# Kernel tuning notes

Hardware: AMD Instinct MI355X
Metric: run time of the kernel (lower is better)

## Reference

```python
import jax, jax.numpy as jnp
import numpy as np

DIM = 512
HEADS = 16
HIDDEN = 2048
EPS = 1e-5


def _layernorm(x, g, b):
    mu = jnp.mean(x, axis=-1, keepdims=True)
    var = jnp.mean((x - mu) ** 2, axis=-1, keepdims=True)
    return (x - mu) * jax.lax.rsqrt(var + EPS) * g + b


def _heads_merge(o):
    # Faithful to source: sum.reshape(B, N, D) applied to [B, H, N, pd]
    # WITHOUT transposing heads back (reproduces the original bug).
    B, H, N, pd = o.shape
    return o.reshape(B, N, H * pd)


def _self_attn(x, w, b, H):
    B, N, D = x.shape
    pd = D // H
    qkv = (x @ w + b).reshape(B, N, 3, H, pd).transpose(2, 0, 3, 1, 4)
    q, k, v = qkv[0], qkv[1], qkv[2]
    # NOTE: no 1/sqrt(pd) scaling in the source.
    s = jax.nn.softmax(jnp.einsum('bhnd,bhmd->bhnm', q, k), axis=-1)
    o = jnp.einsum('bhnm,bhmd->bhnd', s, v)  # == broadcast-multiply-and-sum in source
    return _heads_merge(o)


def _cross_attn(x1, x2, qw, qb, kvw, kvb, H):
    B, N, D = x1.shape
    pd = D // H
    q = (x2 @ qw + qb).reshape(B, N, H, pd).transpose(0, 2, 1, 3)
    kv = (x1 @ kvw + kvb).reshape(B, N, 2, H, pd).transpose(2, 0, 3, 1, 4)
    k, v = kv[0], kv[1]
    s = jax.nn.softmax(jnp.einsum('bhnd,bhmd->bhnm', q, k), axis=-1)
    o = jnp.einsum('bhnm,bhmd->bhnd', s, v)
    return _heads_merge(o)


def setup_inputs() -> dict:
    key = jax.random.key(0)
    ks = jax.random.split(key, 16)
    B, N, D, Hd = 4, 2048, DIM, HIDDEN
    s = 0.02
    return {
        'x1': jax.random.normal(ks[0], (B, N, D), jnp.float32),
        'x2': jax.random.normal(ks[1], (B, N, D), jnp.float32),
        'qkv_w': jax.random.normal(ks[2], (D, 3 * D), jnp.float32) * s,
        'qkv_b': jnp.zeros((3 * D,), jnp.float32),
        'q_w': jax.random.normal(ks[3], (D, D), jnp.float32) * s,
        'q_b': jnp.zeros((D,), jnp.float32),
        'kv_w': jax.random.normal(ks[4], (D, 2 * D), jnp.float32) * s,
        'kv_b': jnp.zeros((2 * D,), jnp.float32),
        'norm_g': jnp.ones((D,), jnp.float32),
        'norm_b': jnp.zeros((D,), jnp.float32),
        'fc1_w': jax.random.normal(ks[5], (D, Hd), jnp.float32) * s,
        'fc1_b': jnp.zeros((Hd,), jnp.float32),
        'fc2_w': jax.random.normal(ks[6], (Hd, D), jnp.float32) * s,
        'fc2_b': jnp.zeros((D,), jnp.float32),
    }


def reference(x1, x2, qkv_w, qkv_b, q_w, q_b, kv_w, kv_b, norm_g, norm_b,
              fc1_w, fc1_b, fc2_w, fc2_b):
    # CrossSelfDecoder.forward
    x = x2 + _cross_attn(x1, x2, q_w, q_b, kv_w, kv_b, HEADS)
    n = _layernorm(x, norm_g, norm_b)  # same norm params reused (as in source)
    x = n + _self_attn(n, qkv_w, qkv_b, HEADS)
    n = _layernorm(x, norm_g, norm_b)
    h = jax.nn.gelu(n @ fc1_w + fc1_b, approximate=False)
    x = n + (h @ fc2_w + fc2_b)
    return x
```

## Files before the change

kernel.cpp:

```cpp
#include <hip/hip_runtime.h>
#include <math.h>

#define DIM 512
#define HEADS 16
#define PD 32
#define NSEQ 2048
#define BATCH 4
#define HIDDEN 2048
#define LOG2E 1.44269504088896f

typedef __attribute__((ext_vector_type(8))) __bf16 bf16x8;
typedef __attribute__((ext_vector_type(4))) float f32x4;
typedef __attribute__((ext_vector_type(16))) float f32x16;

__device__ __forceinline__ ushort f2bf(float f) {
    unsigned u = __float_as_uint(f);
    u = (u + 0x7FFFu + ((u >> 16) & 1u)) >> 16;
    return (ushort)u;
}

__device__ __forceinline__ unsigned cvtpk_bf16(float lo, float hi) {
    unsigned r;
    asm("v_cvt_pk_bf16_f32 %0, %1, %2" : "=v"(r) : "v"(lo), "v"(hi));
    return r;
}

__device__ __forceinline__ float exp2_fast(float x) {
    float r;
    asm("v_exp_f32 %0, %1" : "=v"(r) : "v"(x));
    return r;
}

typedef __attribute__((address_space(1))) const unsigned int g_u32;
typedef __attribute__((address_space(3))) unsigned int l_u32;
__device__ __forceinline__ void gload16(const void* g, void* l) {
    __builtin_amdgcn_global_load_lds((g_u32*)g, (l_u32*)l, 16, 0, 0);
}

__device__ __forceinline__ float gelu_exact(float v) {
    return 0.5f * v * (1.0f + erff(v * 0.70710678118654752f));
}

__global__ __launch_bounds__(256)
void tr_all_kernel(const float* __restrict__ q_w, const float* __restrict__ kv_w,
                   const float* __restrict__ qkv_w, const float* __restrict__ fc1_w,
                   const float* __restrict__ fc2_w, ushort* __restrict__ wtb,
                   const float* __restrict__ x1, const float* __restrict__ x2,
                   ushort* __restrict__ x1b, ushort* __restrict__ x2b)
{
    const int bid = blockIdx.x;
    if (bid >= 3584) {
        int cb = bid - 3584;
        const float* src = (cb < 2048) ? x1 : x2;
        ushort* dst = (cb < 2048) ? x1b : x2b;
        size_t base = (size_t)(cb & 2047) * 2048 + threadIdx.x * 8;
        float4 f0 = *(const float4*)&src[base];
        float4 f1 = *(const float4*)&src[base + 4];
        union { ushort u[8]; uint4 v; } t;
        t.u[0] = f2bf(f0.x); t.u[1] = f2bf(f0.y); t.u[2] = f2bf(f0.z); t.u[3] = f2bf(f0.w);
        t.u[4] = f2bf(f1.x); t.u[5] = f2bf(f1.y); t.u[6] = f2bf(f1.z); t.u[7] = f2bf(f1.w);
        *(uint4*)&dst[base] = t.v;
        return;
    }
    __shared__ float t[32][33];
    const float* W; ushort* Wt; int K, N, lb;
    if (bid < 256)       { W = q_w;   Wt = wtb;           K = 512;  N = 512;  lb = bid; }
    else if (bid < 768)  { W = kv_w;  Wt = wtb + 262144;  K = 512;  N = 1024; lb = bid - 256; }
    else if (bid < 1536) { W = qkv_w; Wt = wtb + 786432;  K = 512;  N = 1536; lb = bid - 768; }
    else if (bid < 2560) { W = fc1_w; Wt = wtb + 1572864; K = 512;  N = 2048; lb = bid - 1536; }
    else                 { W = fc2_w; Wt = wtb + 2621440; K = 2048; N = 512;  lb = bid - 2560; }
    const int nx = N / 32;
    const int n0 = (lb % nx) * 32, k0 = (lb / nx) * 32;
    const int tid = threadIdx.x;
    const int c = tid & 31, r0 = tid >> 5;
    #pragma unroll
    for (int i = 0; i < 4; ++i) {
        int r = r0 + i * 8;
        t[r][c] = W[(size_t)(k0 + r) * N + n0 + c];
    }
    __syncthreads();
    #pragma unroll
    for (int i = 0; i < 4; ++i) {
        int r = r0 + i * 8;
        Wt[(size_t)(n0 + r) * K + k0 + c] = f2bf(t[c][r]);
    }
}

template<int EPI, int NT>
__global__ __launch_bounds__(256)
void mgemm_bf(const ushort* __restrict__ Ap, const ushort* __restrict__ Bt,
              const float* __restrict__ bias, const float* __restrict__ resp,
              void* __restrict__ Cp, ushort* __restrict__ vtp,
              int M, int K, int Nc, int qcols, int vcol0)
{
    const int BN = 32 * NT;
    __shared__ __align__(16) ushort As[2][128 * 32];
    __shared__ __align__(16) ushort Bs[2][BN * 32];

    const int tid = threadIdx.x;
    const int wid = tid >> 6, ln = tid & 63;
    const int g = ln >> 4, c = ln & 15;
    const int wr = wid >> 1, wc = wid & 1;

    const int nwg = gridDim.x * gridDim.y;
    const int lid = blockIdx.y * gridDim.x + blockIdx.x;
    const int wg  = (lid & 7) * (nwg >> 3) + (lid >> 3);
    const int by = wg / gridDim.x, bx = wg % gridDim.x;
    const int row0 = by * 128, col0 = bx * BN;

    const f32x4 fzero = {0.f, 0.f, 0.f, 0.f};
    f32x4 acc[4][NT];
    #pragma unroll
    for (int i = 0; i < 4; ++i)
        #pragma unroll
        for (int j = 0; j < NT; ++j) acc[i][j] = fzero;

    const ushort* asrc[2];
    const ushort* bsrc[NT / 2];
    #pragma unroll
    for (int i = 0; i < 2; ++i) {
        int p = i * 256 + wid * 64 + ln;
        int row = p >> 2;
        int q4 = (p & 3) ^ ((row >> 1) & 3);
        asrc[i] = Ap + (size_t)(row0 + row) * K + q4 * 8;
    }
    #pragma unroll
    for (int i = 0; i < NT / 2; ++i) {
        int p = i * 256 + wid * 64 + ln;
        int row = p >> 2;
        int q4 = (p & 3) ^ ((row >> 1) & 3);
        bsrc[i] = Bt + (size_t)(col0 + row) * K + q4 * 8;
    }

    auto gstage = [&](int bi, int kk) {
        #pragma unroll
        for (int i = 0; i < 2; ++i)
            gload16(asrc[i] + kk, &As[bi][(i * 256 + wid * 64) * 8]);
        #pragma unroll
        for (int i = 0; i < NT / 2; ++i)
            gload16(bsrc[i] + kk, &Bs[bi][(i * 256 + wid * 64) * 8]);
    };

    const int ps = (c >> 1) & 3;
    const int nk = K / 32;

    gstage(0, 0);

    for (int ks = 0; ks < nk; ++ks) {
        __syncthreads();
        if (ks + 1 < nk) gstage((ks + 1) & 1, (ks + 1) * 32);
        const ushort* Ab = As[ks & 1];
        const ushort* Bb = Bs[ks & 1];

        bf16x8 a[4], b[NT];
        #pragma unroll
        for (int mt = 0; mt < 4; ++mt)
            a[mt] = *(const bf16x8*)&Ab[(wr * 64 + mt * 16 + c) * 32 + ((g ^ ps) * 8)];
        #pragma unroll
        for (int nt = 0; nt < NT; ++nt)
            b[nt] = *(const bf16x8*)&Bb[(wc * (16 * NT) + nt * 16 + c) * 32 + ((g ^ ps) * 8)];

        #pragma unroll
        for (int mt = 0; mt < 4; ++mt)
            #pragma unroll
            for (int nt = 0; nt < NT; ++nt)
                acc[mt][nt] = __builtin_amdgcn_mfma_f32_16x16x32_bf16(a[mt], b[nt], acc[mt][nt], 0, 0, 0);
    }

    float bs[NT];
    #pragma unroll
    for (int nt = 0; nt < NT; ++nt) bs[nt] = bias[col0 + wc * (16 * NT) + nt * 16 + c];

    #pragma unroll
    for (int mt = 0; mt < 4; ++mt) {
        const int rb = row0 + wr * 64 + mt * 16 + g * 4;
        #pragma unroll
        for (int nt = 0; nt < NT; ++nt) {
            const int col = col0 + wc * (16 * NT) + nt * 16 + c;
            if (EPI == 3 && col >= vcol0) {
                int cc = col - vcol0;
                int hh = cc >> 5, pd = cc & 31;
                int bq = rb >> 11, ntok = rb & 2047;
                union { ushort u[4]; uint2 v; } pk;
                #pragma unroll
                for (int reg = 0; reg < 4; ++reg)
                    pk.u[reg] = f2bf(acc[mt][nt][reg] + bs[nt]);
                *(uint2*)&vtp[((size_t)(bq * 16 + hh) * 32 + pd) * 2048 + ntok] = pk.v;
            } else {
                #pragma unroll
                for (int reg = 0; reg < 4; ++reg) {
                    int r = rb + reg;
                    float v = acc[mt][nt][reg] + bs[nt];
                    if (EPI == 1) {
                        ((ushort*)Cp)[(size_t)r * Nc + col] = f2bf(gelu_exact(v));
                    } else if (EPI == 2) {
                        ((float*)Cp)[(size_t)r * Nc + col] = v + resp[(size_t)r * Nc + col];
                    } else {
                        float v2 = (col < qcols) ? v * LOG2E : v;
                        ((ushort*)Cp)[(size_t)r * Nc + col] = f2bf(v2);
                    }
                }
            }
        }
    }
}

__global__ __launch_bounds__(256)
void attn_mfma_kernel(const ushort* __restrict__ qb_, int qstride, int qoff,
                      const ushort* __restrict__ kb_, int kstride, int koff,
                      const ushort* __restrict__ vtg,
                      const float* res, const float* __restrict__ gptr,
                      const float* __restrict__ bptr,
                      float* nf32, ushort* __restrict__ nb16)
{
    __shared__ __align__(16) ushort Klds[2][128 * 32];
    __shared__ __align__(16) ushort Vtlds[2][32 * 128];

    const int tid = threadIdx.x;
    const int w   = tid >> 6;
    const int ln  = tid & 63;
    const int c32 = ln & 31;
    const int hi  = ln >> 5;

    const int bid = blockIdx.x;
    const int xcd = bid & 7, jj = bid >> 3;
    const int bh = xcd + 8 * (jj >> 4);
    const int qt = jj & 15;
    const int b = bh >> 4, h = bh & 15;
    const size_t rowbase = (size_t)b * NSEQ;
    const int qt0 = qt * 128 + w * 32;
    const int n = qt0 + c32;

    bf16x8 qfrag[2];
    #pragma unroll
    for (int ph = 0; ph < 2; ++ph)
        qfrag[ph] = *(const bf16x8*)(qb_ + (rowbase + n) * qstride + qoff
                                     + h * PD + ph * 16 + hi * 8);

    const ushort* ks[2];
    const ushort* vs[2];
    int kd[2], vd[2];
    #pragma unroll
    for (int i = 0; i < 2; ++i) {
        int ch = 2 * w + i;
        int kvc = ch * 16 + (ln >> 2);
        int q4  = (ln & 3) ^ ((kvc >> 1) & 3);
        ks[i] = kb_ + (rowbase + kvc) * kstride + koff + h * PD + q4 * 8;
        kd[i] = ch * 512;
        int pdc = ch * 4 + (ln >> 4);
        int kv0 = ((ln & 15) ^ (pdc & 15)) * 8;
        vs[i] = vtg + ((size_t)bh * PD + pdc) * 2048 + kv0;
        vd[i] = ch * 512;
    }

#define STAGE(bi, trow)                                              \
    {                                                                \
        gload16(ks[0] + (size_t)(trow) * kstride, &Klds[bi][kd[0]]); \
        gload16(ks[1] + (size_t)(trow) * kstride, &Klds[bi][kd[1]]); \
        gload16(vs[0] + (trow), &Vtlds[bi][vd[0]]);                  \
        gload16(vs[1] + (trow), &Vtlds[bi][vd[1]]);                  \
    }

    f32x16 oacc, zero16;
    #pragma unroll
    for (int i = 0; i < 16; ++i) { oacc[i] = 0.f; zero16[i] = 0.f; }
    float l = 0.f;

    STAGE(0, 0);

    for (int t = 0; t < NSEQ / 128; ++t) {
        __syncthreads();
        if (t < NSEQ / 128 - 1) STAGE((t + 1) & 1, (t + 1) * 128);
        const ushort* Kb = Klds[t & 1];
        const ushort* Vb = Vtlds[t & 1];

        #pragma unroll
        for (int hh = 0; hh < 2; ++hh) {
            bf16x8 kf[2][2];
            #pragma unroll
            for (int kt = 0; kt < 2; ++kt)
                #pragma unroll
                for (int ph = 0; ph < 2; ++ph) {
                    int slot = (2 * ph + hi) ^ ((c32 >> 1) & 3);
                    kf[kt][ph] = *(const bf16x8*)&Kb[(hh * 64 + kt * 32 + c32) * 32 + slot * 8];
                }
            bf16x8 vf[4];
            #pragma unroll
            for (int j = 0; j < 4; ++j) {
                int slot = (hh * 8 + 2 * j + hi) ^ (c32 & 15);
                vf[j] = *(const bf16x8*)&Vb[c32 * 128 + slot * 8];
            }

            f32x16 st[2];
            __builtin_amdgcn_s_setprio(1);
            #pragma unroll
            for (int kt = 0; kt < 2; ++kt) {
                st[kt] = __builtin_amdgcn_mfma_f32_32x32x16_bf16(kf[kt][0], qfrag[0], zero16, 0, 0, 0);
                st[kt] = __builtin_amdgcn_mfma_f32_32x32x16_bf16(kf[kt][1], qfrag[1], st[kt], 0, 0, 0);
            }
            __builtin_amdgcn_s_setprio(0);

            float r0 = 0.f, r1 = 0.f, r2 = 0.f, r3 = 0.f;
            #pragma unroll
            for (int kt = 0; kt < 2; ++kt) {
                #pragma unroll
                for (int i = 0; i < 4; ++i) {
                    float p0 = exp2_fast(st[kt][i * 4 + 0]);
                    float p1 = exp2_fast(st[kt][i * 4 + 1]);
                    float p2 = exp2_fast(st[kt][i * 4 + 2]);
                    float p3 = exp2_fast(st[kt][i * 4 + 3]);
                    st[kt][i * 4 + 0] = p0; r0 += p0;
                    st[kt][i * 4 + 1] = p1; r1 += p1;
                    st[kt][i * 4 + 2] = p2; r2 += p2;
                    st[kt][i * 4 + 3] = p3; r3 += p3;
                }
            }
            float rsum = (r0 + r1) + (r2 + r3);
            rsum += __shfl_xor(rsum, 32);
            l += rsum;

            unsigned wpk[2][4][2];
            #pragma unroll
            for (int kt = 0; kt < 2; ++kt)
                #pragma unroll
                for (int rg = 0; rg < 4; ++rg) {
                    wpk[kt][rg][0] = cvtpk_bf16(st[kt][rg * 4 + 0], st[kt][rg * 4 + 1]);
                    wpk[kt][rg][1] = cvtpk_bf16(st[kt][rg * 4 + 2], st[kt][rg * 4 + 3]);
                }

            __builtin_amdgcn_s_setprio(1);
            #pragma unroll
            for (int j = 0; j < 4; ++j) {
                int kt = j >> 1, rg0 = 2 * (j & 1);
                unsigned x0 = wpk[kt][rg0][0], y0 = wpk[kt][rg0 + 1][0];
                unsigned x1 = wpk[kt][rg0][1], y1 = wpk[kt][rg0 + 1][1];
                asm("v_permlane32_swap_b32 %0, %1" : "+v"(x0), "+v"(y0));
                asm("v_permlane32_swap_b32 %0, %1" : "+v"(x1), "+v"(y1));
                union { unsigned u[4]; bf16x8 v; } pf;
                pf.u[0] = x0; pf.u[1] = x1; pf.u[2] = y0; pf.u[3] = y1;
                oacc = __builtin_amdgcn_mfma_f32_32x32x16_bf16(vf[j], pf.v, oacc, 0, 0, 0);
            }
            __builtin_amdgcn_s_setprio(0);
        }
    }
#undef STAGE

    const float inv = 1.0f / l;
    const int row2 = h * 128 + (n >> 4);
    const int colb = (n & 15) * PD;
    const size_t rowoff = (rowbase + row2) * DIM;

    float xv[16];
    float s = 0.f, ss = 0.f;
    #pragma unroll
    for (int ch = 0; ch < 4; ++ch) {
        float4 r4 = *(const float4*)&res[rowoff + colb + ch * 8 + hi * 4];
        #pragma unroll
        for (int q = 0; q < 4; ++q) {
            float rv = (q == 0) ? r4.x : (q == 1) ? r4.y : (q == 2) ? r4.z : r4.w;
            float x = rv + oacc[ch * 4 + q] * inv;
            xv[ch * 4 + q] = x; s += x; ss += x * x;
        }
    }
    s += __shfl_xor(s, 1);  ss += __shfl_xor(ss, 1);
    s += __shfl_xor(s, 2);  ss += __shfl_xor(ss, 2);
    s += __shfl_xor(s, 4);  ss += __shfl_xor(ss, 4);
    s += __shfl_xor(s, 8);  ss += __shfl_xor(ss, 8);
    s += __shfl_xor(s, 32); ss += __shfl_xor(ss, 32);
    float mu = s * (1.0f / DIM);
    float var = ss * (1.0f / DIM) - mu * mu;
    float rr = rsqrtf(var + 1e-5f);

    #pragma unroll
    for (int ch = 0; ch < 4; ++ch) {
        const int off = colb + ch * 8 + hi * 4;
        float4 g4 = *(const float4*)&gptr[off];
        float4 b4 = *(const float4*)&bptr[off];
        float y0 = (xv[ch * 4 + 0] - mu) * rr * g4.x + b4.x;
        float y1 = (xv[ch * 4 + 1] - mu) * rr * g4.y + b4.y;
        float y2 = (xv[ch * 4 + 2] - mu) * rr * g4.z + b4.z;
        float y3 = (xv[ch * 4 + 3] - mu) * rr * g4.w + b4.w;
        float4 yv = {y0, y1, y2, y3};
        *(float4*)&nf32[rowoff + off] = yv;
        uint2 pk = {cvtpk_bf16(y0, y1), cvtpk_bf16(y2, y3)};
        *(uint2*)&nb16[rowoff + off] = pk;
    }
}

extern "C" void kernel_launch(void* const* d_in, const int* in_sizes, int n_in,
                              void* d_out, int out_size, void* d_ws, size_t ws_size,
                              hipStream_t stream)
{
    const float* x1     = (const float*)d_in[0];
    const float* x2     = (const float*)d_in[1];
    const float* qkv_w  = (const float*)d_in[2];
    const float* qkv_b  = (const float*)d_in[3];
    const float* q_w    = (const float*)d_in[4];
    const float* q_b    = (const float*)d_in[5];
    const float* kv_w   = (const float*)d_in[6];
    const float* kv_b   = (const float*)d_in[7];
    const float* norm_g = (const float*)d_in[8];
    const float* norm_b = (const float*)d_in[9];
    const float* fc1_w  = (const float*)d_in[10];
    const float* fc1_b  = (const float*)d_in[11];
    const float* fc2_w  = (const float*)d_in[12];
    const float* fc2_b  = (const float*)d_in[13];
    float* out = (float*)d_out;
    float* ws  = (float*)d_ws;

    const int M = BATCH * NSEQ;
    const int BIG = 1 << 30;

    ushort* wtb    = (ushort*)ws;
    ushort* q_wt   = wtb;
    ushort* kv_wt  = wtb + 262144;
    ushort* qkv_wt = wtb + 786432;
    ushort* fc1_wt = wtb + 1572864;
    ushort* fc2_wt = wtb + 2621440;
    ushort* proj_u = (ushort*)(ws + (size_t)2 * 1024 * 1024);
    ushort* kvb16  = proj_u;
    ushort* qb16   = proj_u + (size_t)8192 * 1024;
    ushort* qkvb16 = proj_u;
    ushort* hbuf   = proj_u;
    ushort* VtG    = (ushort*)(ws + (size_t)21 * 512 * 1024);
    float*  n1f32  = ws + (size_t)13 * 1024 * 1024;
    ushort* n1b16  = (ushort*)(ws + (size_t)17 * 1024 * 1024);
    ushort* n2b16  = (ushort*)(ws + (size_t)19 * 1024 * 1024);
    ushort* x1b    = n1b16;
    ushort* x2b    = n2b16;

    dim3 blk(256);

    tr_all_kernel<<<dim3(7680), blk, 0, stream>>>(
        q_w, kv_w, qkv_w, fc1_w, fc2_w, wtb, x1, x2, x1b, x2b);

    mgemm_bf<3, 4><<<dim3(1024 / 128, M / 128), blk, 0, stream>>>(
        x1b, kv_wt, kv_b, nullptr, kvb16, VtG, M, DIM, 1024, 0, 512);
    mgemm_bf<3, 2><<<dim3(512 / 64, M / 128), blk, 0, stream>>>(
        x2b, q_wt, q_b, nullptr, qb16, nullptr, M, DIM, 512, 512, BIG);
    attn_mfma_kernel<<<dim3(1024), blk, 0, stream>>>(
        qb16, 512, 0, kvb16, 1024, 0, VtG, x2, norm_g, norm_b, n1f32, n1b16);

    mgemm_bf<3, 4><<<dim3(1536 / 128, M / 128), blk, 0, stream>>>(
        n1b16, qkv_wt, qkv_b, nullptr, qkvb16, VtG, M, DIM, 1536, 512, 1024);
    attn_mfma_kernel<<<dim3(1024), blk, 0, stream>>>(
        qkvb16, 1536, 0, qkvb16, 1536, 512, VtG, n1f32, norm_g, norm_b, n1f32, n2b16);

    mgemm_bf<1, 4><<<dim3(HIDDEN / 128, M / 128), blk, 0, stream>>>(
        n2b16, fc1_wt, fc1_b, nullptr, hbuf, nullptr, M, DIM, HIDDEN, 0, BIG);
    mgemm_bf<2, 2><<<dim3(512 / 64, M / 128), blk, 0, stream>>>(
        hbuf, fc2_wt, fc2_b, n1f32, out, nullptr, M, HIDDEN, DIM, 0, BIG);
}
```

Before: 274.2 us.

## Split attention over two KV halves and merge with separate layernorm kernel

```diff
diff --git a/kernel.cpp b/kernel.cpp
--- a/kernel.cpp
+++ b/kernel.cpp
@@ -17,6 +17,10 @@
     unsigned u = __float_as_uint(f);
     u = (u + 0x7FFFu + ((u >> 16) & 1u)) >> 16;
     return (ushort)u;
+}
+
+__device__ __forceinline__ float bf2f(ushort u) {
+    return __uint_as_float(((unsigned)u) << 16);
 }
 
 __device__ __forceinline__ unsigned cvtpk_bf16(float lo, float hi) {
@@ -206,12 +210,10 @@
 }
 
 __global__ __launch_bounds__(256)
-void attn_mfma_kernel(const ushort* __restrict__ qb_, int qstride, int qoff,
+void attn_part_kernel(const ushort* __restrict__ qb_, int qstride, int qoff,
                       const ushort* __restrict__ kb_, int kstride, int koff,
                       const ushort* __restrict__ vtg,
-                      const float* res, const float* __restrict__ gptr,
-                      const float* __restrict__ bptr,
-                      float* nf32, ushort* __restrict__ nb16)
+                      ushort* __restrict__ opart, float* __restrict__ lpart)
 {
     __shared__ __align__(16) ushort Klds[2][128 * 32];
     __shared__ __align__(16) ushort Vtlds[2][32 * 128];
@@ -223,13 +225,19 @@
     const int hi  = ln >> 5;
 
     const int bid = blockIdx.x;
-    const int xcd = bid & 7, jj = bid >> 3;
+    const int half = bid >> 10;
+    const int sb = bid & 1023;
+    const int xcd = sb & 7, jj = sb >> 3;
     const int bh = xcd + 8 * (jj >> 4);
     const int qt = jj & 15;
     const int b = bh >> 4, h = bh & 15;
     const size_t rowbase = (size_t)b * NSEQ;
     const int qt0 = qt * 128 + w * 32;
     const int n = qt0 + c32;
+    const int t0base = half * (NSEQ / 2);
+
+    ushort* oph = opart + (size_t)half * 8192 * 512;
+    float*  lph = lpart + (size_t)half * 64 * 2048;
 
     bf16x8 qfrag[2];
     #pragma unroll
@@ -245,11 +253,11 @@
         int ch = 2 * w + i;
         int kvc = ch * 16 + (ln >> 2);
         int q4  = (ln & 3) ^ ((kvc >> 1) & 3);
-        ks[i] = kb_ + (rowbase + kvc) * kstride + koff + h * PD + q4 * 8;
+        ks[i] = kb_ + (rowbase + t0base + kvc) * kstride + koff + h * PD + q4 * 8;
         kd[i] = ch * 512;
         int pdc = ch * 4 + (ln >> 4);
         int kv0 = ((ln & 15) ^ (pdc & 15)) * 8;
-        vs[i] = vtg + ((size_t)bh * PD + pdc) * 2048 + kv0;
+        vs[i] = vtg + ((size_t)bh * PD + pdc) * 2048 + t0base + kv0;
         vd[i] = ch * 512;
     }
 
@@ -268,9 +276,9 @@
 
     STAGE(0, 0);
 
-    for (int t = 0; t < NSEQ / 128; ++t) {
+    for (int t = 0; t < NSEQ / 256; ++t) {
         __syncthreads();
-        if (t < NSEQ / 128 - 1) STAGE((t + 1) & 1, (t + 1) * 128);
+        if (t < NSEQ / 256 - 1) STAGE((t + 1) & 1, (t + 1) * 128);
         const ushort* Kb = Klds[t & 1];
         const ushort* Vb = Vtlds[t & 1];
 
@@ -345,46 +353,85 @@
     }
 #undef STAGE
 
-    const float inv = 1.0f / l;
     const int row2 = h * 128 + (n >> 4);
     const int colb = (n & 15) * PD;
     const size_t rowoff = (rowbase + row2) * DIM;
-
-    float xv[16];
+    #pragma unroll
+    for (int ch = 0; ch < 4; ++ch) {
+        const int off = colb + ch * 8 + hi * 4;
+        uint2 pk = {cvtpk_bf16(oacc[ch * 4 + 0], oacc[ch * 4 + 1]),
+                    cvtpk_bf16(oacc[ch * 4 + 2], oacc[ch * 4 + 3])};
+        *(uint2*)&oph[rowoff + off] = pk;
+    }
+    if (hi == 0) lph[(size_t)bh * 2048 + n] = l;
+}
+
+__global__ __launch_bounds__(256)
+void merge_ln_kernel(const ushort* __restrict__ opart, const float* __restrict__ lpart,
+                     const float* __restrict__ res, const float* __restrict__ gptr,
+                     const float* __restrict__ bptr,
+                     float* __restrict__ nf32, ushort* __restrict__ nb16)
+{
+    const int w = threadIdx.x >> 6, ln = threadIdx.x & 63;
+    const int r = blockIdx.x * 4 + w;
+    const int b = r >> 11, row2 = r & 2047, h = row2 >> 7;
+    const int col0 = ln * 8;
+    const int nn = (row2 & 127) * 16 + (col0 >> 5);
+    const size_t li = (size_t)(b * 16 + h) * 2048 + nn;
+    const float inv = 1.0f / (lpart[li] + lpart[li + 64 * 2048]);
+    const size_t oi = (size_t)r * 512 + col0;
+
+    uint4 o1 = *(const uint4*)&opart[oi];
+    uint4 o2 = *(const uint4*)&opart[oi + (size_t)8192 * 512];
+    float4 rs0 = *(const float4*)&res[oi];
+    float4 rs1 = *(const float4*)&res[oi + 4];
+
+    float x[8];
+    const unsigned* u1 = (const unsigned*)&o1;
+    const unsigned* u2 = (const unsigned*)&o2;
+    #pragma unroll
+    for (int j = 0; j < 4; ++j) {
+        float a0 = bf2f((ushort)(u1[j] & 0xFFFF)) + bf2f((ushort)(u2[j] & 0xFFFF));
+        float a1 = bf2f((ushort)(u1[j] >> 16))    + bf2f((ushort)(u2[j] >> 16));
+        float rv0 = (j < 2) ? ((j == 0) ? rs0.x : rs0.z) : ((j == 2) ? rs1.x : rs1.z);
+        float rv1 = (j < 2) ? ((j == 0) ? rs0.y : rs0.w) : ((j == 2) ? rs1.y : rs1.w);
+        x[j * 2 + 0] = rv0 + a0 * inv;
+        x[j * 2 + 1] = rv1 + a1 * inv;
+    }
+
     float s = 0.f, ss = 0.f;
     #pragma unroll
-    for (int ch = 0; ch < 4; ++ch) {
-        float4 r4 = *(const float4*)&res[rowoff + colb + ch * 8 + hi * 4];
-        #pragma unroll
-        for (int q = 0; q < 4; ++q) {
-            float rv = (q == 0) ? r4.x : (q == 1) ? r4.y : (q == 2) ? r4.z : r4.w;
-            float x = rv + oacc[ch * 4 + q] * inv;
-            xv[ch * 4 + q] = x; s += x; ss += x * x;
-        }
-    }
-    s += __shfl_xor(s, 1);  ss += __shfl_xor(ss, 1);
-    s += __shfl_xor(s, 2);  ss += __shfl_xor(ss, 2);
-    s += __shfl_xor(s, 4);  ss += __shfl_xor(ss, 4);
-    s += __shfl_xor(s, 8);  ss += __shfl_xor(ss, 8);
-    s += __shfl_xor(s, 32); ss += __shfl_xor(ss, 32);
+    for (int j = 0; j < 8; ++j) { s += x[j]; ss += x[j] * x[j]; }
+    #pragma unroll
+    for (int off = 1; off <= 32; off <<= 1) {
+        s  += __shfl_xor(s, off);
+        ss += __shfl_xor(ss, off);
+    }
     float mu = s * (1.0f / DIM);
     float var = ss * (1.0f / DIM) - mu * mu;
     float rr = rsqrtf(var + 1e-5f);
 
-    #pragma unroll
-    for (int ch = 0; ch < 4; ++ch) {
-        const int off = colb + ch * 8 + hi * 4;
-        float4 g4 = *(const float4*)&gptr[off];
-        float4 b4 = *(const float4*)&bptr[off];
-        float y0 = (xv[ch * 4 + 0] - mu) * rr * g4.x + b4.x;
-        float y1 = (xv[ch * 4 + 1] - mu) * rr * g4.y + b4.y;
-        float y2 = (xv[ch * 4 + 2] - mu) * rr * g4.z + b4.z;
-        float y3 = (xv[ch * 4 + 3] - mu) * rr * g4.w + b4.w;
-        float4 yv = {y0, y1, y2, y3};
-        *(float4*)&nf32[rowoff + off] = yv;
-        uint2 pk = {cvtpk_bf16(y0, y1), cvtpk_bf16(y2, y3)};
-        *(uint2*)&nb16[rowoff + off] = pk;
-    }
+    float4 g0 = *(const float4*)&gptr[col0];
+    float4 g1 = *(const float4*)&gptr[col0 + 4];
+    float4 b0 = *(const float4*)&bptr[col0];
+    float4 b1 = *(const float4*)&bptr[col0 + 4];
+    float y[8];
+    y[0] = (x[0] - mu) * rr * g0.x + b0.x;
+    y[1] = (x[1] - mu) * rr * g0.y + b0.y;
+    y[2] = (x[2] - mu) * rr * g0.z + b0.z;
+    y[3] = (x[3] - mu) * rr * g0.w + b0.w;
+    y[4] = (x[4] - mu) * rr * g1.x + b1.x;
+    y[5] = (x[5] - mu) * rr * g1.y + b1.y;
+    y[6] = (x[6] - mu) * rr * g1.z + b1.z;
+    y[7] = (x[7] - mu) * rr * g1.w + b1.w;
+
+    float4 yv0 = {y[0], y[1], y[2], y[3]};
+    float4 yv1 = {y[4], y[5], y[6], y[7]};
+    *(float4*)&nf32[oi]     = yv0;
+    *(float4*)&nf32[oi + 4] = yv1;
+    uint4 pk = {cvtpk_bf16(y[0], y[1]), cvtpk_bf16(y[2], y[3]),
+                cvtpk_bf16(y[4], y[5]), cvtpk_bf16(y[6], y[7])};
+    *(uint4*)&nb16[oi] = pk;
 }
 
 extern "C" void kernel_launch(void* const* d_in, const int* in_sizes, int n_in,
@@ -423,9 +470,11 @@
     ushort* qkvb16 = proj_u;
     ushort* hbuf   = proj_u;
     ushort* VtG    = (ushort*)(ws + (size_t)21 * 512 * 1024);
+    float*  lpart  = ws + (size_t)25 * 512 * 1024;
     float*  n1f32  = ws + (size_t)13 * 1024 * 1024;
     ushort* n1b16  = (ushort*)(ws + (size_t)17 * 1024 * 1024);
     ushort* n2b16  = (ushort*)(ws + (size_t)19 * 1024 * 1024);
+    ushort* opart  = (ushort*)(ws + (size_t)21 * 1024 * 1024);
     ushort* x1b    = n1b16;
     ushort* x2b    = n2b16;
 
@@ -438,13 +487,17 @@
         x1b, kv_wt, kv_b, nullptr, kvb16, VtG, M, DIM, 1024, 0, 512);
     mgemm_bf<3, 2><<<dim3(512 / 64, M / 128), blk, 0, stream>>>(
         x2b, q_wt, q_b, nullptr, qb16, nullptr, M, DIM, 512, 512, BIG);
-    attn_mfma_kernel<<<dim3(1024), blk, 0, stream>>>(
-        qb16, 512, 0, kvb16, 1024, 0, VtG, x2, norm_g, norm_b, n1f32, n1b16);
+    attn_part_kernel<<<dim3(2048), blk, 0, stream>>>(
+        qb16, 512, 0, kvb16, 1024, 0, VtG, opart, lpart);
+    merge_ln_kernel<<<dim3(M / 4), blk, 0, stream>>>(
+        opart, lpart, x2, norm_g, norm_b, n1f32, n1b16);
 
     mgemm_bf<3, 4><<<dim3(1536 / 128, M / 128), blk, 0, stream>>>(
         n1b16, qkv_wt, qkv_b, nullptr, qkvb16, VtG, M, DIM, 1536, 512, 1024);
-    attn_mfma_kernel<<<dim3(1024), blk, 0, stream>>>(
-        qkvb16, 1536, 0, qkvb16, 1536, 512, VtG, n1f32, norm_g, norm_b, n1f32, n2b16);
+    attn_part_kernel<<<dim3(2048), blk, 0, stream>>>(
+        qkvb16, 1536, 0, qkvb16, 1536, 512, VtG, opart, lpart);
+    merge_ln_kernel<<<dim3(M / 4), blk, 0, stream>>>(
+        opart, lpart, n1f32, norm_g, norm_b, n1f32, n2b16);
 
     mgemm_bf<1, 4><<<dim3(HIDDEN / 128, M / 128), blk, 0, stream>>>(
         n2b16, fc1_wt, fc1_b, nullptr, hbuf, nullptr, M, DIM, HIDDEN, 0, BIG);
```

Result: no change. 277.8 us (+1.3%).

## Split attention KV range across two blocks with atomic last-block combine

Applied to the files above, without the earlier changes.

```diff
diff --git a/kernel.cpp b/kernel.cpp
--- a/kernel.cpp
+++ b/kernel.cpp
@@ -19,6 +19,10 @@
     return (ushort)u;
 }
 
+__device__ __forceinline__ float bf2f(ushort u) {
+    return __uint_as_float(((unsigned)u) << 16);
+}
+
 __device__ __forceinline__ unsigned cvtpk_bf16(float lo, float hi) {
     unsigned r;
     asm("v_cvt_pk_bf16_f32 %0, %1, %2" : "=v"(r) : "v"(lo), "v"(hi));
@@ -46,9 +50,18 @@
                    const float* __restrict__ qkv_w, const float* __restrict__ fc1_w,
                    const float* __restrict__ fc2_w, ushort* __restrict__ wtb,
                    const float* __restrict__ x1, const float* __restrict__ x2,
-                   ushort* __restrict__ x1b, ushort* __restrict__ x2b)
+                   ushort* __restrict__ x1b, ushort* __restrict__ x2b,
+                   unsigned* __restrict__ ctr)
 {
     const int bid = blockIdx.x;
+    if (bid == 7680) {
+        uint2 z = {0u, 0u};
+        *(uint2*)&ctr[threadIdx.x * 8]     = z;
+        *(uint2*)&ctr[threadIdx.x * 8 + 2] = z;
+        *(uint2*)&ctr[threadIdx.x * 8 + 4] = z;
+        *(uint2*)&ctr[threadIdx.x * 8 + 6] = z;
+        return;
+    }
     if (bid >= 3584) {
         int cb = bid - 3584;
         const float* src = (cb < 2048) ? x1 : x2;
@@ -206,9 +219,11 @@
 }
 
 __global__ __launch_bounds__(256)
-void attn_mfma_kernel(const ushort* __restrict__ qb_, int qstride, int qoff,
+void attn_part_kernel(const ushort* __restrict__ qb_, int qstride, int qoff,
                       const ushort* __restrict__ kb_, int kstride, int koff,
                       const ushort* __restrict__ vtg,
+                      ushort* __restrict__ opart, float* __restrict__ lpart,
+                      unsigned* __restrict__ ctr,
                       const float* res, const float* __restrict__ gptr,
                       const float* __restrict__ bptr,
                       float* nf32, ushort* __restrict__ nb16)
@@ -223,13 +238,19 @@
     const int hi  = ln >> 5;
 
     const int bid = blockIdx.x;
-    const int xcd = bid & 7, jj = bid >> 3;
+    const int half = bid >> 10;
+    const int sb = bid & 1023;
+    const int xcd = sb & 7, jj = sb >> 3;
     const int bh = xcd + 8 * (jj >> 4);
     const int qt = jj & 15;
     const int b = bh >> 4, h = bh & 15;
     const size_t rowbase = (size_t)b * NSEQ;
     const int qt0 = qt * 128 + w * 32;
     const int n = qt0 + c32;
+    const int t0base = half * (NSEQ / 2);
+
+    ushort* oph = opart + (size_t)half * 8192 * 512;
+    float*  lph = lpart + (size_t)half * 64 * 2048;
 
     bf16x8 qfrag[2];
     #pragma unroll
@@ -245,11 +266,11 @@
         int ch = 2 * w + i;
         int kvc = ch * 16 + (ln >> 2);
         int q4  = (ln & 3) ^ ((kvc >> 1) & 3);
-        ks[i] = kb_ + (rowbase + kvc) * kstride + koff + h * PD + q4 * 8;
+        ks[i] = kb_ + (rowbase + t0base + kvc) * kstride + koff + h * PD + q4 * 8;
         kd[i] = ch * 512;
         int pdc = ch * 4 + (ln >> 4);
         int kv0 = ((ln & 15) ^ (pdc & 15)) * 8;
-        vs[i] = vtg + ((size_t)bh * PD + pdc) * 2048 + kv0;
+        vs[i] = vtg + ((size_t)bh * PD + pdc) * 2048 + t0base + kv0;
         vd[i] = ch * 512;
     }
 
@@ -268,9 +289,9 @@
 
     STAGE(0, 0);
 
-    for (int t = 0; t < NSEQ / 128; ++t) {
+    for (int t = 0; t < NSEQ / 256; ++t) {
         __syncthreads();
-        if (t < NSEQ / 128 - 1) STAGE((t + 1) & 1, (t + 1) * 128);
+        if (t < NSEQ / 256 - 1) STAGE((t + 1) & 1, (t + 1) * 128);
         const ushort* Kb = Klds[t & 1];
         const ushort* Vb = Vtlds[t & 1];
 
@@ -345,22 +366,48 @@
     }
 #undef STAGE
 
-    const float inv = 1.0f / l;
     const int row2 = h * 128 + (n >> 4);
     const int colb = (n & 15) * PD;
     const size_t rowoff = (rowbase + row2) * DIM;
-
+    #pragma unroll
+    for (int ch = 0; ch < 4; ++ch) {
+        const int off = colb + ch * 8 + hi * 4;
+        uint2 pk = {cvtpk_bf16(oacc[ch * 4 + 0], oacc[ch * 4 + 1]),
+                    cvtpk_bf16(oacc[ch * 4 + 2], oacc[ch * 4 + 3])};
+        *(uint2*)&oph[rowoff + off] = pk;
+    }
+    if (hi == 0) lph[(size_t)bh * 2048 + n] = l;
+
+    __threadfence();
+    __syncthreads();
+    int* flag = (int*)&Klds[0][0];
+    if (tid == 0) flag[0] = (int)atomicAdd(&ctr[sb], 1u);
+    __syncthreads();
+    if (flag[0] != 1) return;
+    __threadfence();
+
+    const float linv = 1.0f / (lpart[(size_t)bh * 2048 + n]
+                               + lpart[(size_t)64 * 2048 + (size_t)bh * 2048 + n]);
     float xv[16];
     float s = 0.f, ss = 0.f;
     #pragma unroll
     for (int ch = 0; ch < 4; ++ch) {
-        float4 r4 = *(const float4*)&res[rowoff + colb + ch * 8 + hi * 4];
-        #pragma unroll
-        for (int q = 0; q < 4; ++q) {
-            float rv = (q == 0) ? r4.x : (q == 1) ? r4.y : (q == 2) ? r4.z : r4.w;
-            float x = rv + oacc[ch * 4 + q] * inv;
-            xv[ch * 4 + q] = x; s += x; ss += x * x;
-        }
+        const int off = colb + ch * 8 + hi * 4;
+        uint2 a = *(const uint2*)&opart[rowoff + off];
+        uint2 b2 = *(const uint2*)&opart[(size_t)8192 * 512 + rowoff + off];
+        float4 r4 = *(const float4*)&res[rowoff + off];
+        float e0 = bf2f((ushort)(a.x & 0xFFFF)) + bf2f((ushort)(b2.x & 0xFFFF));
+        float e1 = bf2f((ushort)(a.x >> 16))    + bf2f((ushort)(b2.x >> 16));
+        float e2 = bf2f((ushort)(a.y & 0xFFFF)) + bf2f((ushort)(b2.y & 0xFFFF));
+        float e3 = bf2f((ushort)(a.y >> 16))    + bf2f((ushort)(b2.y >> 16));
+        float x0 = r4.x + e0 * linv;
+        float x1 = r4.y + e1 * linv;
+        float x2v = r4.z + e2 * linv;
+        float x3 = r4.w + e3 * linv;
+        xv[ch * 4 + 0] = x0; xv[ch * 4 + 1] = x1;
+        xv[ch * 4 + 2] = x2v; xv[ch * 4 + 3] = x3;
+        s += (x0 + x1) + (x2v + x3);
+        ss += (x0 * x0 + x1 * x1) + (x2v * x2v + x3 * x3);
     }
     s += __shfl_xor(s, 1);  ss += __shfl_xor(ss, 1);
     s += __shfl_xor(s, 2);  ss += __shfl_xor(ss, 2);
@@ -423,28 +470,33 @@
     ushort* qkvb16 = proj_u;
     ushort* hbuf   = proj_u;
     ushort* VtG    = (ushort*)(ws + (size_t)21 * 512 * 1024);
+    float*  lpart  = ws + (size_t)25 * 512 * 1024;
+    unsigned* ctr  = (unsigned*)(ws + (size_t)51 * 256 * 1024);
     float*  n1f32  = ws + (size_t)13 * 1024 * 1024;
     ushort* n1b16  = (ushort*)(ws + (size_t)17 * 1024 * 1024);
     ushort* n2b16  = (ushort*)(ws + (size_t)19 * 1024 * 1024);
+    ushort* opart  = (ushort*)(ws + (size_t)21 * 1024 * 1024);
     ushort* x1b    = n1b16;
     ushort* x2b    = n2b16;
 
     dim3 blk(256);
 
-    tr_all_kernel<<<dim3(7680), blk, 0, stream>>>(
-        q_w, kv_w, qkv_w, fc1_w, fc2_w, wtb, x1, x2, x1b, x2b);
+    tr_all_kernel<<<dim3(7681), blk, 0, stream>>>(
+        q_w, kv_w, qkv_w, fc1_w, fc2_w, wtb, x1, x2, x1b, x2b, ctr);
 
     mgemm_bf<3, 4><<<dim3(1024 / 128, M / 128), blk, 0, stream>>>(
         x1b, kv_wt, kv_b, nullptr, kvb16, VtG, M, DIM, 1024, 0, 512);
     mgemm_bf<3, 2><<<dim3(512 / 64, M / 128), blk, 0, stream>>>(
         x2b, q_wt, q_b, nullptr, qb16, nullptr, M, DIM, 512, 512, BIG);
-    attn_mfma_kernel<<<dim3(1024), blk, 0, stream>>>(
-        qb16, 512, 0, kvb16, 1024, 0, VtG, x2, norm_g, norm_b, n1f32, n1b16);
+    attn_part_kernel<<<dim3(2048), blk, 0, stream>>>(
+        qb16, 512, 0, kvb16, 1024, 0, VtG, opart, lpart, ctr,
+        x2, norm_g, norm_b, n1f32, n1b16);
 
     mgemm_bf<3, 4><<<dim3(1536 / 128, M / 128), blk, 0, stream>>>(
         n1b16, qkv_wt, qkv_b, nullptr, qkvb16, VtG, M, DIM, 1536, 512, 1024);
-    attn_mfma_kernel<<<dim3(1024), blk, 0, stream>>>(
-        qkvb16, 1536, 0, qkvb16, 1536, 512, VtG, n1f32, norm_g, norm_b, n1f32, n2b16);
+    attn_part_kernel<<<dim3(2048), blk, 0, stream>>>(
+        qkvb16, 1536, 0, qkvb16, 1536, 512, VtG, opart, lpart, ctr + 1024,
+        n1f32, norm_g, norm_b, n1f32, n2b16);
 
     mgemm_bf<1, 4><<<dim3(HIDDEN / 128, M / 128), blk, 0, stream>>>(
         n2b16, fc1_wt, fc1_b, nullptr, hbuf, nullptr, M, DIM, HIDDEN, 0, BIG);
```

After: 1.013 ms. 3.7x slower.

## Give each wave private K/V LDS buffers to drop block-wide barriers in attention

Applied to the files above, without the earlier changes.

```diff
diff --git a/kernel.cpp b/kernel.cpp
--- a/kernel.cpp
+++ b/kernel.cpp
@@ -213,8 +213,7 @@
                       const float* __restrict__ bptr,
                       float* nf32, ushort* __restrict__ nb16)
 {
-    __shared__ __align__(16) ushort Klds[2][128 * 32];
-    __shared__ __align__(16) ushort Vtlds[2][32 * 128];
+    __shared__ __align__(16) ushort AllLds[4][4096];
 
     const int tid = threadIdx.x;
     const int w   = tid >> 6;
@@ -228,37 +227,35 @@
     const int qt = jj & 15;
     const int b = bh >> 4, h = bh & 15;
     const size_t rowbase = (size_t)b * NSEQ;
-    const int qt0 = qt * 128 + w * 32;
-    const int n = qt0 + c32;
+    const int n = qt * 128 + w * 32 + c32;
+
+    ushort* Kw = &AllLds[w][0];
+    ushort* Vw = &AllLds[w][2048];
 
     bf16x8 qfrag[2];
     #pragma unroll
     for (int ph = 0; ph < 2; ++ph)
         qfrag[ph] = *(const bf16x8*)(qb_ + (rowbase + n) * qstride + qoff
                                      + h * PD + ph * 16 + hi * 8);
-
-    const ushort* ks[2];
-    const ushort* vs[2];
-    int kd[2], vd[2];
+    asm volatile("s_waitcnt vmcnt(0)" ::: "memory");
+
+    const ushort* ksrc[2];
+    const ushort* vsrc[2];
     #pragma unroll
     for (int i = 0; i < 2; ++i) {
-        int ch = 2 * w + i;
-        int kvc = ch * 16 + (ln >> 2);
-        int q4  = (ln & 3) ^ ((kvc >> 1) & 3);
-        ks[i] = kb_ + (rowbase + kvc) * kstride + koff + h * PD + q4 * 8;
-        kd[i] = ch * 512;
-        int pdc = ch * 4 + (ln >> 4);
-        int kv0 = ((ln & 15) ^ (pdc & 15)) * 8;
-        vs[i] = vtg + ((size_t)bh * PD + pdc) * 2048 + kv0;
-        vd[i] = ch * 512;
-    }
-
-#define STAGE(bi, trow)                                              \
-    {                                                                \
-        gload16(ks[0] + (size_t)(trow) * kstride, &Klds[bi][kd[0]]); \
-        gload16(ks[1] + (size_t)(trow) * kstride, &Klds[bi][kd[1]]); \
-        gload16(vs[0] + (trow), &Vtlds[bi][vd[0]]);                  \
-        gload16(vs[1] + (trow), &Vtlds[bi][vd[1]]);                  \
+        int p = i * 64 + ln;
+        int row = p >> 2;
+        int q4 = (p & 3) ^ ((row >> 1) & 3);
+        ksrc[i] = kb_ + (rowbase + row) * kstride + koff + h * PD + q4 * 8;
+        vsrc[i] = vtg + ((size_t)bh * PD + row) * 2048 + q4 * 8;
+    }
+
+#define STAGE(bi, t0)                                                     \
+    {                                                                     \
+        gload16(ksrc[0] + (size_t)(t0) * kstride, &Kw[(bi) * 1024]);      \
+        gload16(ksrc[1] + (size_t)(t0) * kstride, &Kw[(bi) * 1024 + 512]);\
+        gload16(vsrc[0] + (t0), &Vw[(bi) * 1024]);                        \
+        gload16(vsrc[1] + (t0), &Vw[(bi) * 1024 + 512]);                  \
     }
 
     f32x16 oacc, zero16;
@@ -266,82 +263,70 @@
     for (int i = 0; i < 16; ++i) { oacc[i] = 0.f; zero16[i] = 0.f; }
     float l = 0.f;
 
+    const int sA = (c32 >> 1) & 3;
+
     STAGE(0, 0);
 
-    for (int t = 0; t < NSEQ / 128; ++t) {
-        __syncthreads();
-        if (t < NSEQ / 128 - 1) STAGE((t + 1) & 1, (t + 1) * 128);
-        const ushort* Kb = Klds[t & 1];
-        const ushort* Vb = Vtlds[t & 1];
-
-        #pragma unroll
-        for (int hh = 0; hh < 2; ++hh) {
-            bf16x8 kf[2][2];
-            #pragma unroll
-            for (int kt = 0; kt < 2; ++kt)
-                #pragma unroll
-                for (int ph = 0; ph < 2; ++ph) {
-                    int slot = (2 * ph + hi) ^ ((c32 >> 1) & 3);
-                    kf[kt][ph] = *(const bf16x8*)&Kb[(hh * 64 + kt * 32 + c32) * 32 + slot * 8];
-                }
-            bf16x8 vf[4];
-            #pragma unroll
-            for (int j = 0; j < 4; ++j) {
-                int slot = (hh * 8 + 2 * j + hi) ^ (c32 & 15);
-                vf[j] = *(const bf16x8*)&Vb[c32 * 128 + slot * 8];
-            }
-
-            f32x16 st[2];
-            __builtin_amdgcn_s_setprio(1);
-            #pragma unroll
-            for (int kt = 0; kt < 2; ++kt) {
-                st[kt] = __builtin_amdgcn_mfma_f32_32x32x16_bf16(kf[kt][0], qfrag[0], zero16, 0, 0, 0);
-                st[kt] = __builtin_amdgcn_mfma_f32_32x32x16_bf16(kf[kt][1], qfrag[1], st[kt], 0, 0, 0);
-            }
-            __builtin_amdgcn_s_setprio(0);
-
-            float r0 = 0.f, r1 = 0.f, r2 = 0.f, r3 = 0.f;
-            #pragma unroll
-            for (int kt = 0; kt < 2; ++kt) {
-                #pragma unroll
-                for (int i = 0; i < 4; ++i) {
-                    float p0 = exp2_fast(st[kt][i * 4 + 0]);
-                    float p1 = exp2_fast(st[kt][i * 4 + 1]);
-                    float p2 = exp2_fast(st[kt][i * 4 + 2]);
-                    float p3 = exp2_fast(st[kt][i * 4 + 3]);
-                    st[kt][i * 4 + 0] = p0; r0 += p0;
-                    st[kt][i * 4 + 1] = p1; r1 += p1;
-                    st[kt][i * 4 + 2] = p2; r2 += p2;
-                    st[kt][i * 4 + 3] = p3; r3 += p3;
-                }
-            }
-            float rsum = (r0 + r1) + (r2 + r3);
-            rsum += __shfl_xor(rsum, 32);
-            l += rsum;
-
-            unsigned wpk[2][4][2];
-            #pragma unroll
-            for (int kt = 0; kt < 2; ++kt)
-                #pragma unroll
-                for (int rg = 0; rg < 4; ++rg) {
-                    wpk[kt][rg][0] = cvtpk_bf16(st[kt][rg * 4 + 0], st[kt][rg * 4 + 1]);
-                    wpk[kt][rg][1] = cvtpk_bf16(st[kt][rg * 4 + 2], st[kt][rg * 4 + 3]);
-                }
-
-            __builtin_amdgcn_s_setprio(1);
-            #pragma unroll
-            for (int j = 0; j < 4; ++j) {
-                int kt = j >> 1, rg0 = 2 * (j & 1);
-                unsigned x0 = wpk[kt][rg0][0], y0 = wpk[kt][rg0 + 1][0];
-                unsigned x1 = wpk[kt][rg0][1], y1 = wpk[kt][rg0 + 1][1];
-                asm("v_permlane32_swap_b32 %0, %1" : "+v"(x0), "+v"(y0));
-                asm("v_permlane32_swap_b32 %0, %1" : "+v"(x1), "+v"(y1));
-                union { unsigned u[4]; bf16x8 v; } pf;
-                pf.u[0] = x0; pf.u[1] = x1; pf.u[2] = y0; pf.u[3] = y1;
-                oacc = __builtin_amdgcn_mfma_f32_32x32x16_bf16(vf[j], pf.v, oacc, 0, 0, 0);
-            }
-            __builtin_amdgcn_s_setprio(0);
-        }
+    for (int t = 0; t < NSEQ / 32; ++t) {
+        __builtin_amdgcn_sched_barrier(0);
+        if (t + 1 < NSEQ / 32) {
+            STAGE((t + 1) & 1, (t + 1) * 32);
+            asm volatile("s_waitcnt vmcnt(4)" ::: "memory");
+        } else {
+            asm volatile("s_waitcnt vmcnt(0)" ::: "memory");
+        }
+        __builtin_amdgcn_sched_barrier(0);
+
+        const ushort* Kb = &Kw[(t & 1) * 1024];
+        const ushort* Vb = &Vw[(t & 1) * 1024];
+
+        bf16x8 kf[2];
+        #pragma unroll
+        for (int ph = 0; ph < 2; ++ph)
+            kf[ph] = *(const bf16x8*)&Kb[c32 * 32 + (((2 * ph + hi) ^ sA) * 8)];
+        bf16x8 vf[2];
+        #pragma unroll
+        for (int j = 0; j < 2; ++j)
+            vf[j] = *(const bf16x8*)&Vb[c32 * 32 + (((2 * j + hi) ^ sA) * 8)];
+
+        f32x16 st;
+        __builtin_amdgcn_s_setprio(1);
+        st = __builtin_amdgcn_mfma_f32_32x32x16_bf16(kf[0], qfrag[0], zero16, 0, 0, 0);
+        st = __builtin_amdgcn_mfma_f32_32x32x16_bf16(kf[1], qfrag[1], st, 0, 0, 0);
+        __builtin_amdgcn_s_setprio(0);
+
+        float r0 = 0.f, r1 = 0.f;
+        #pragma unroll
+        for (int i = 0; i < 8; ++i) {
+            float p0 = exp2_fast(st[i * 2 + 0]);
+            float p1 = exp2_fast(st[i * 2 + 1]);
+            st[i * 2 + 0] = p0; r0 += p0;
+            st[i * 2 + 1] = p1; r1 += p1;
+        }
+        float rsum = r0 + r1;
+        rsum += __shfl_xor(rsum, 32);
+        l += rsum;
+
+        unsigned wpk[4][2];
+        #pragma unroll
+        for (int rg = 0; rg < 4; ++rg) {
+            wpk[rg][0] = cvtpk_bf16(st[rg * 4 + 0], st[rg * 4 + 1]);
+            wpk[rg][1] = cvtpk_bf16(st[rg * 4 + 2], st[rg * 4 + 3]);
+        }
+
+        __builtin_amdgcn_s_setprio(1);
+        #pragma unroll
+        for (int j = 0; j < 2; ++j) {
+            int rg0 = 2 * j;
+            unsigned x0 = wpk[rg0][0], y0 = wpk[rg0 + 1][0];
+            unsigned x1 = wpk[rg0][1], y1 = wpk[rg0 + 1][1];
+            asm("v_permlane32_swap_b32 %0, %1" : "+v"(x0), "+v"(y0));
+            asm("v_permlane32_swap_b32 %0, %1" : "+v"(x1), "+v"(y1));
+            union { unsigned u[4]; bf16x8 v; } pf;
+            pf.u[0] = x0; pf.u[1] = x1; pf.u[2] = y0; pf.u[3] = y1;
+            oacc = __builtin_amdgcn_mfma_f32_32x32x16_bf16(vf[j], pf.v, oacc, 0, 0, 0);
+        }
+        __builtin_amdgcn_s_setprio(0);
     }
 #undef STAGE
 
```

Measured after the change: 302.8 us. 1.1x slower.
